# Kernel tuning notes

Hardware: AMD Instinct MI355X
Metric: run time of the kernel (lower is better)

The kernel has to match this reference:

```python
import jax, jax.numpy as jnp
import numpy as np
from jax import lax

AGG_HOPS = 3
RANK_K = 10
NEG = -1e9


def _aggregate(embs, agg_w, agg_b, W_last, b_last):
    # GIKT-style multi-hop mean aggregation: embs[j] has shape [B, n1..nj, D]
    embs = list(embs)
    for i in range(AGG_HOPS):
        for j in range(AGG_HOPS - i):
            s = jnp.mean(embs[j + 1], axis=-2) + embs[j]
            embs[j] = jnp.tanh(s @ agg_w[j].T + agg_b[j])
    return jnp.tanh(embs[0] @ W_last.T + b_last)


def _hops(nodes0, tabA, tabB):
    # alternating bipartite neighbor expansion: [B] -> [B,n] -> [B,n,n] -> ...
    lst = [nodes0]
    for i in range(AGG_HOPS):
        tab = tabA if i % 2 == 0 else tabB
        lst.append(tab[lst[-1]])
    return lst


def _forward(user, question, response, mask, q_neighbors, s_neighbors, u_neighbors,
             q_neighbors_2, qs_index, emb_question, emb_question_2, emb_skill,
             emb_user, emb_response, w1_q, w2_q, W_ih, W_hh, b_ih, b_hh,
             agg_w, agg_b, W_agg_last, b_agg_last, W_query, b_query, W_key, b_key,
             W_w, b_w, W_fusion, b_fusion):
    B, T = question.shape
    D = emb_question.shape[1]
    emb_q_all = emb_question[question]  # [B,T,D], used for recap similarity
    wA, wB = W_w[0, :D], W_w[0, D:]     # MLP_W(cat(Q,K)) = Q@wA + K@wB + b

    def predict(qs_concat, states, svalid):
        ql = (qs_concat @ W_query.T + b_query) @ wA          # [B,Lq]
        kl = (states @ W_key.T + b_key) @ wB                 # [B,Ls]
        logit = ql[:, :, None] + kl[:, None, :] + b_w[0]     # [B,Lq,Ls]
        logit = jnp.where(svalid[:, None, :], logit, NEG)
        Lq, Ls = logit.shape[1], logit.shape[2]
        alpha = jax.nn.softmax(logit.reshape(B, -1), axis=1).reshape(B, Lq, Ls)
        g = jnp.einsum('bqd,bsd->bqs', qs_concat, states)
        return jax.nn.sigmoid(jnp.sum(alpha * g, axis=(1, 2)))

    def step(carry, t):
        h, c, sh = carry
        q_t, u_t, r_t = question[:, t], user[:, t], response[:, t]
        m = (mask[:, t] == 1)[:, None]  # [B,1]
        # question-skill GNN branch
        embs_q = [(emb_question if i % 2 == 0 else emb_skill)[n]
                  for i, n in enumerate(_hops(q_t, q_neighbors, s_neighbors))]
        e1 = jnp.where(m, _aggregate(embs_q, agg_w, agg_b, W_agg_last, b_agg_last),
                       emb_question[q_t])
        # user-question GNN branch
        embs_u = [(emb_user if i % 2 == 0 else emb_question_2)[n]
                  for i, n in enumerate(_hops(u_t, u_neighbors, q_neighbors_2))]
        e2 = jnp.where(m, _aggregate(embs_u, agg_w, agg_b, W_agg_last, b_agg_last),
                       emb_question_2[q_t])
        e_hat = w1_q * e1 + w2_q * e2
        e_t = jax.nn.relu(jnp.concatenate([e_hat, emb_response[r_t]], axis=1)
                          @ W_fusion.T + b_fusion)
        # masked LSTMCell (torch gate order i,f,g,o); dropout in eval mode
        gates = e_t @ W_ih.T + b_ih + h @ W_hh.T + b_hh
        gi, gf, gg, go = jnp.split(gates, 4, axis=1)
        c2 = jax.nn.sigmoid(gf) * c + jax.nn.sigmoid(gi) * jnp.tanh(gg)
        h2 = jax.nn.sigmoid(go) * jnp.tanh(c2)
        h = jnp.where(m, h2, h)
        c = jnp.where(m, c2, c)
        sh = lax.dynamic_update_slice(sh, h[:, None, :], (0, t, 0))
        # next question + its related skills
        q_next = question[:, t + 1]
        emb_qn = emb_question[q_next]
        qs_concat = jnp.concatenate([emb_qn[:, None, :], emb_skill[qs_index[q_next]]], axis=1)
        # soft recap: top-k past states by (detached) question similarity
        scores = lax.stop_gradient(jnp.einsum('btd,bd->bt', emb_q_all, emb_qn))
        valid_t = jnp.arange(T) < t
        scores = jnp.where(valid_t[None, :], scores, NEG)
        _, idx = lax.top_k(scores, RANK_K)                    # [B,K]
        sel = jnp.take_along_axis(sh, idx[:, :, None], axis=1)  # [B,K,D]
        svalid = jnp.concatenate([jnp.ones((B, 1), bool), valid_t[idx]], axis=1)
        states = jnp.concatenate([h[:, None, :], sel], axis=1)  # [B,1+K,D]
        y = predict(qs_concat, states, svalid)
        return (h, c, sh), y

    h0 = jnp.zeros((B, D), jnp.float32)
    sh0 = jnp.zeros((B, T, D), jnp.float32)
    _, ys = lax.scan(step, (h0, h0, sh0), jnp.arange(T - 1))
    return jnp.concatenate([jnp.full((B, 1), 0.5, jnp.float32), ys.T], axis=1)


def setup_inputs() -> dict:
    B, T, D = 32, 50, 100
    NQ, NS, NU = 20000, 500, 10000
    NBR, SPQ = 6, 4
    key = jax.random.key(0)
    ks = iter(jax.random.split(key, 48))
    nrm = lambda shape, sc: jax.random.normal(next(ks), shape, jnp.float32) * sc
    ri = lambda shape, hi: jax.random.randint(next(ks), shape, 0, hi, jnp.int32)
    s = 1.0 / float(np.sqrt(D))
    return {
        'user': ri((B, T), NU), 'question': ri((B, T), NQ),
        'response': ri((B, T), 2), 'mask': ri((B, T), 2),
        'q_neighbors': ri((NQ, NBR), NS), 's_neighbors': ri((NS, NBR), NQ),
        'u_neighbors': ri((NU, NBR), NQ), 'q_neighbors_2': ri((NQ, NBR), NU),
        'qs_index': ri((NQ, SPQ), NS),
        'emb_question': nrm((NQ, D), 0.1), 'emb_question_2': nrm((NQ, D), 0.1),
        'emb_skill': nrm((NS, D), 0.1), 'emb_user': nrm((NU, D), 0.1),
        'emb_response': nrm((2, D), 0.1),
        'w1_q': jnp.float32(0.5), 'w2_q': jnp.float32(0.5),
        'W_ih': nrm((4 * D, D), s), 'W_hh': nrm((4 * D, D), s),
        'b_ih': jnp.zeros((4 * D,), jnp.float32), 'b_hh': jnp.zeros((4 * D,), jnp.float32),
        'agg_w': nrm((3, D, D), s), 'agg_b': jnp.zeros((3, D), jnp.float32),
        'W_agg_last': nrm((D, D), s), 'b_agg_last': jnp.zeros((D,), jnp.float32),
        'W_query': nrm((D, D), s), 'b_query': jnp.zeros((D,), jnp.float32),
        'W_key': nrm((D, D), s), 'b_key': jnp.zeros((D,), jnp.float32),
        'W_w': nrm((1, 2 * D), s), 'b_w': jnp.zeros((1,), jnp.float32),
        'W_fusion': nrm((D, 2 * D), s), 'b_fusion': jnp.zeros((D,), jnp.float32),
    }


def reference(user, question, response, mask, q_neighbors, s_neighbors, u_neighbors,
              q_neighbors_2, qs_index, emb_question, emb_question_2, emb_skill,
              emb_user, emb_response, w1_q, w2_q, W_ih, W_hh, b_ih, b_hh,
              agg_w, agg_b, W_agg_last, b_agg_last, W_query, b_query, W_key, b_key,
              W_w, b_w, W_fusion, b_fusion):
    return _forward(user, question, response, mask, q_neighbors, s_neighbors,
                    u_neighbors, q_neighbors_2, qs_index, emb_question,
                    emb_question_2, emb_skill, emb_user, emb_response, w1_q, w2_q,
                    W_ih, W_hh, b_ih, b_hh, agg_w, agg_b, W_agg_last, b_agg_last,
                    W_query, b_query, W_key, b_key, W_w, b_w, W_fusion, b_fusion)
```

## Files before the change

kernel.cpp:

```cpp
#include <hip/hip_runtime.h>
#include <hip/hip_bf16.h>

#define BSZ 32
#define TT 50
#define TS 49
#define PH 108

#define OFF_GPRE  0u
#define OFF_QL    627200u
#define OFF_IDX   639744u
#define OFF_NV    655424u
#define OFF_QSC   656992u
#define OFF_E1    1440992u
#define OFF_E2    1597792u

#define RLF(v,l) __uint_as_float(__builtin_amdgcn_readlane(__float_as_uint(v), (l)))

__device__ __forceinline__ float tanh_fast(float x) {
    float e = __expf(2.f * x);
    return 1.f - __fdividef(2.f, e + 1.f);
}
__device__ __forceinline__ float sigm_fast(float x) {
    return __fdividef(1.f, 1.f + __expf(-x));
}
__device__ __forceinline__ float dot4(float4 a, float4 b) {
    return a.x*b.x + a.y*b.y + a.z*b.z + a.w*b.w;
}

__global__ __launch_bounds__(256, 2) void kagg(
    const int* __restrict__ user, const int* __restrict__ question, const int* __restrict__ mask,
    const int* __restrict__ qnbr, const int* __restrict__ snbr,
    const int* __restrict__ unbr, const int* __restrict__ qnbr2,
    const float* __restrict__ embQ, const float* __restrict__ embQ2, const float* __restrict__ embS,
    const float* __restrict__ embU,
    const float* __restrict__ aggw, const float* __restrict__ aggb,
    const float* __restrict__ wlast, const float* __restrict__ blast,
    float* __restrict__ WS)
{
    int bid = blockIdx.x;
    int tid = threadIdx.x;

    int pair = bid >> 1, which = bid & 1;
    int b = pair / TS, t = pair - b*TS;
    int mm = mask[b*TT + t];
    float* outE = WS + (which ? OFF_E2 : OFF_E1) + (size_t)pair*100;

    if (mm != 1) {
        int q_t = question[b*TT + t];
        const float4* src = (const float4*)((which ? embQ2 : embQ) + (size_t)q_t*100);
        if (tid < 25) ((float4*)outE)[tid] = src[tid];
        return;
    }

    int root = which ? user[b*TT + t] : question[b*TT + t];
    const int*   tabA = which ? unbr  : qnbr;
    const int*   tabB = which ? qnbr2 : snbr;
    const float4* eE = (const float4*)(which ? embU  : embQ);
    const float4* eO = (const float4*)(which ? embQ2 : embS);

    __shared__ __align__(16) float b2in[36*108];
    __shared__ __align__(16) float x1[6*108];
    __shared__ float s2v1b[600];
    __shared__ float v1a[600];
    __shared__ __align__(16) float x0[104], v0a[104], v0b[104];
    __shared__ int n1[8], n2[36], n3[216];

    if (tid < 6) n1[tid] = tabA[root*6 + tid];
    __syncthreads();
    if (tid < 36) n2[tid] = tabB[n1[tid/6]*6 + (tid % 6)];
    __syncthreads();
    if (tid < 216) n3[tid] = tabA[n2[tid/6]*6 + (tid % 6)];
    __syncthreads();
    for (int i4 = tid; i4 < 900; i4 += 256) {
        int v = i4 / 25, j = i4 - v*25;
        float4 a = eE[(size_t)n2[v]*25 + j];
        float4 s = make_float4(0.f, 0.f, 0.f, 0.f);
        const int* p = n3 + v*6;
        #pragma unroll
        for (int c = 0; c < 6; ++c) {
            float4 o = eO[(size_t)p[c]*25 + j];
            s.x += o.x; s.y += o.y; s.z += o.z; s.w += o.w;
        }
        float4 r = make_float4(a.x + s.x*(1.f/6.f), a.y + s.y*(1.f/6.f),
                               a.z + s.z*(1.f/6.f), a.w + s.w*(1.f/6.f));
        *(float4*)(b2in + v*108 + 4*j) = r;
    }
    for (int i4 = tid; i4 < 150; i4 += 256) {
        int a = i4 / 25, j = i4 - a*25;
        float4 base = eO[(size_t)n1[a]*25 + j];
        float4 s = make_float4(0.f, 0.f, 0.f, 0.f);
        #pragma unroll
        for (int c = 0; c < 6; ++c) {
            float4 o = eE[(size_t)n2[a*6 + c]*25 + j];
            s.x += o.x; s.y += o.y; s.z += o.z; s.w += o.w;
        }
        float4 r = make_float4(base.x + s.x*(1.f/6.f), base.y + s.y*(1.f/6.f),
                               base.z + s.z*(1.f/6.f), base.w + s.w*(1.f/6.f));
        *(float4*)(x1 + a*108 + 4*j) = r;
    }
    if (tid >= 160 && tid < 185) {
        int j = tid - 160;
        float4 base = eE[(size_t)root*25 + j];
        float4 s = make_float4(0.f, 0.f, 0.f, 0.f);
        #pragma unroll
        for (int a = 0; a < 6; ++a) {
            float4 o = eO[(size_t)n1[a]*25 + j];
            s.x += o.x; s.y += o.y; s.z += o.z; s.w += o.w;
        }
        float4 r = make_float4(base.x + s.x*(1.f/6.f), base.y + s.y*(1.f/6.f),
                               base.z + s.z*(1.f/6.f), base.w + s.w*(1.f/6.f));
        *(float4*)(x0 + 4*j) = r;
    }
    __syncthreads();
    if (tid < 150) {
        int dblk = tid / 6, a = tid - dblk*6, d0 = dblk*4;
        const float* wp = aggw + 20000 + d0*100;
        const float* xb = b2in + a*648;
        float acc[4][6];
        #pragma unroll
        for (int r = 0; r < 4; ++r)
            #pragma unroll
            for (int c = 0; c < 6; ++c) acc[r][c] = 0.f;
        #pragma unroll
        for (int j = 0; j < 25; ++j) {
            float4 r0 = *(const float4*)(wp + 4*j);
            float4 r1 = *(const float4*)(wp + 100 + 4*j);
            float4 r2 = *(const float4*)(wp + 200 + 4*j);
            float4 r3 = *(const float4*)(wp + 300 + 4*j);
            #pragma unroll
            for (int c = 0; c < 6; ++c) {
                float4 x = *(const float4*)(xb + c*108 + 4*j);
                acc[0][c] += dot4(r0, x);
                acc[1][c] += dot4(r1, x);
                acc[2][c] += dot4(r2, x);
                acc[3][c] += dot4(r3, x);
            }
        }
        #pragma unroll
        for (int r = 0; r < 4; ++r) {
            float bia = aggb[200 + d0 + r];
            float o = 0.f;
            #pragma unroll
            for (int c = 0; c < 6; ++c) o += tanh_fast(bia + acc[r][c]);
            s2v1b[a*100 + d0 + r] = o;
        }
    } else if (tid >= 160 && tid < 210) {
        int d0 = (tid - 160)*2;
        const float* wp = aggw + 10000 + d0*100;
        float a0[6], a1[6];
        #pragma unroll
        for (int c = 0; c < 6; ++c) { a0[c] = 0.f; a1[c] = 0.f; }
        #pragma unroll
        for (int j = 0; j < 25; ++j) {
            float4 r0 = *(const float4*)(wp + 4*j);
            float4 r1 = *(const float4*)(wp + 100 + 4*j);
            #pragma unroll
            for (int c = 0; c < 6; ++c) {
                float4 x = *(const float4*)(x1 + c*108 + 4*j);
                a0[c] += dot4(r0, x);
                a1[c] += dot4(r1, x);
            }
        }
        #pragma unroll
        for (int c = 0; c < 6; ++c) {
            v1a[c*100 + d0]     = tanh_fast(aggb[100 + d0] + a0[c]);
            v1a[c*100 + d0 + 1] = tanh_fast(aggb[100 + d0 + 1] + a1[c]);
        }
    } else if (tid >= 216 && tid < 241) {
        int d0 = (tid - 216)*4;
        const float* wp = aggw + d0*100;
        float a0 = 0.f, a1 = 0.f, a2 = 0.f, a3 = 0.f;
        #pragma unroll
        for (int j = 0; j < 25; ++j) {
            float4 x = *(const float4*)(x0 + 4*j);
            a0 += dot4(*(const float4*)(wp + 4*j), x);
            a1 += dot4(*(const float4*)(wp + 100 + 4*j), x);
            a2 += dot4(*(const float4*)(wp + 200 + 4*j), x);
            a3 += dot4(*(const float4*)(wp + 300 + 4*j), x);
        }
        v0a[d0]   = tanh_fast(aggb[d0] + a0);
        v0a[d0+1] = tanh_fast(aggb[d0+1] + a1);
        v0a[d0+2] = tanh_fast(aggb[d0+2] + a2);
        v0a[d0+3] = tanh_fast(aggb[d0+3] + a3);
    }
    __syncthreads();
    for (int e = tid; e < 600; e += 256) {
        int a = e / 100, d = e - a*100;
        x1[a*108 + d] = v1a[a*100 + d] + s2v1b[a*100 + d]*(1.f/6.f);
    }
    if (tid >= 128 && tid < 228) {
        int d = tid - 128;
        float s = 0.f;
        #pragma unroll
        for (int a = 0; a < 6; ++a) s += v1a[a*100 + d];
        x0[d] = v0a[d] + s*(1.f/6.f);
    }
    __syncthreads();
    if (tid < 50) {
        int d0 = tid*2;
        const float* wp = aggw + 10000 + d0*100;
        float a0[6], a1[6];
        #pragma unroll
        for (int c = 0; c < 6; ++c) { a0[c] = 0.f; a1[c] = 0.f; }
        #pragma unroll
        for (int j = 0; j < 25; ++j) {
            float4 r0 = *(const float4*)(wp + 4*j);
            float4 r1 = *(const float4*)(wp + 100 + 4*j);
            #pragma unroll
            for (int c = 0; c < 6; ++c) {
                float4 x = *(const float4*)(x1 + c*108 + 4*j);
                a0[c] += dot4(r0, x);
                a1[c] += dot4(r1, x);
            }
        }
        #pragma unroll
        for (int c = 0; c < 6; ++c) {
            s2v1b[c*100 + d0]     = tanh_fast(aggb[100 + d0] + a0[c]);
            s2v1b[c*100 + d0 + 1] = tanh_fast(aggb[100 + d0 + 1] + a1[c]);
        }
    } else if (tid >= 64 && tid < 89) {
        int d0 = (tid - 64)*4;
        const float* wp = aggw + d0*100;
        float a0 = 0.f, a1 = 0.f, a2 = 0.f, a3 = 0.f;
        #pragma unroll
        for (int j = 0; j < 25; ++j) {
            float4 x = *(const float4*)(x0 + 4*j);
            a0 += dot4(*(const float4*)(wp + 4*j), x);
            a1 += dot4(*(const float4*)(wp + 100 + 4*j), x);
            a2 += dot4(*(const float4*)(wp + 200 + 4*j), x);
            a3 += dot4(*(const float4*)(wp + 300 + 4*j), x);
        }
        v0b[d0]   = tanh_fast(aggb[d0] + a0);
        v0b[d0+1] = tanh_fast(aggb[d0+1] + a1);
        v0b[d0+2] = tanh_fast(aggb[d0+2] + a2);
        v0b[d0+3] = tanh_fast(aggb[d0+3] + a3);
    }
    __syncthreads();
    if (tid < 100) {
        float s = 0.f;
        #pragma unroll
        for (int a = 0; a < 6; ++a) s += s2v1b[a*100 + tid];
        x0[tid] = v0b[tid] + s*(1.f/6.f);
    }
    __syncthreads();
    if (tid < 25) {
        int d0 = tid*4;
        const float* wp = aggw + d0*100;
        float a0 = 0.f, a1 = 0.f, a2 = 0.f, a3 = 0.f;
        #pragma unroll
        for (int j = 0; j < 25; ++j) {
            float4 x = *(const float4*)(x0 + 4*j);
            a0 += dot4(*(const float4*)(wp + 4*j), x);
            a1 += dot4(*(const float4*)(wp + 100 + 4*j), x);
            a2 += dot4(*(const float4*)(wp + 200 + 4*j), x);
            a3 += dot4(*(const float4*)(wp + 300 + 4*j), x);
        }
        v0a[d0]   = tanh_fast(aggb[d0] + a0);
        v0a[d0+1] = tanh_fast(aggb[d0+1] + a1);
        v0a[d0+2] = tanh_fast(aggb[d0+2] + a2);
        v0a[d0+3] = tanh_fast(aggb[d0+3] + a3);
    }
    __syncthreads();
    if (tid < 25) {
        int d0 = tid*4;
        const float* wp = wlast + d0*100;
        float a0 = 0.f, a1 = 0.f, a2 = 0.f, a3 = 0.f;
        #pragma unroll
        for (int j = 0; j < 25; ++j) {
            float4 x = *(const float4*)(v0a + 4*j);
            a0 += dot4(*(const float4*)(wp + 4*j), x);
            a1 += dot4(*(const float4*)(wp + 100 + 4*j), x);
            a2 += dot4(*(const float4*)(wp + 200 + 4*j), x);
            a3 += dot4(*(const float4*)(wp + 300 + 4*j), x);
        }
        float4 r = make_float4(tanh_fast(blast[d0] + a0), tanh_fast(blast[d0+1] + a1),
                               tanh_fast(blast[d0+2] + a2), tanh_fast(blast[d0+3] + a3));
        *(float4*)(outE + d0) = r;
    }
}

__global__ __launch_bounds__(256, 2) void kfuse(
    const int* __restrict__ question, const int* __restrict__ response,
    const int* __restrict__ qsidx,
    const float* __restrict__ embQ, const float* __restrict__ embS, const float* __restrict__ embR,
    const float* __restrict__ w1p, const float* __restrict__ w2p,
    const float* __restrict__ wfus, const float* __restrict__ bfus,
    const float* __restrict__ wih, const float* __restrict__ bih, const float* __restrict__ bhh,
    const float* __restrict__ wq, const float* __restrict__ bq, const float* __restrict__ ww,
    float* __restrict__ WS)
{
    int bid = blockIdx.x;
    int b = bid / TS, t = bid - b*TS;
    int tid = threadIdx.x;
    size_t bt = (size_t)b*TS + t;

    __shared__ __align__(16) float sEIN[200], sET[112], sEQN[104], sQSCm[500];
    __shared__ float sWW[104], sVQ[104], sScore[52], sCq[1];

    int r_t = response[b*TT + t];
    int qn  = question[b*TT + t + 1];
    if (tid < 100) {
        sEIN[tid] = w1p[0]*WS[OFF_E1 + bt*100 + tid] + w2p[0]*WS[OFF_E2 + bt*100 + tid];
    } else if (tid < 200) {
        sEIN[tid] = embR[r_t*100 + (tid - 100)];
        if (tid < 150) {
            int d = tid - 100;
            sEQN[d]      = embQ[(size_t)qn*100 + d];
            sEQN[d + 50] = embQ[(size_t)qn*100 + d + 50];
        }
    } else {
        for (int i = tid - 200; i < 100; i += 56) sWW[i] = ww[i];
    }
    __syncthreads();
    if (tid < 160) {
        int slot = tid >> 4, k0 = tid & 15;
        #pragma unroll
        for (int rp = 0; rp < 10; ++rp) {
            int row = rp*10 + slot;
            const float* wr = wfus + row*200;
            float acc = 0.f;
            #pragma unroll
            for (int m = 0; m < 4; ++m) {
                int f4i = k0 + 16*m;
                if (f4i < 50)
                    acc += dot4(*(const float4*)(wr + 4*f4i), *(const float4*)(sEIN + 4*f4i));
            }
            acc += __shfl_xor(acc, 1); acc += __shfl_xor(acc, 2);
            acc += __shfl_xor(acc, 4); acc += __shfl_xor(acc, 8);
            if (k0 == 0) sET[row] = fmaxf(acc + bfus[row], 0.f);
        }
    } else {
        for (int k = tid - 160; k < 100; k += 96) {
            float a = 0.f;
            for (int d = 0; d < 100; ++d) a += sWW[d] * wq[d*100 + k];
            sVQ[k] = a;
        }
        if (tid == 255) {
            float a = 0.f;
            for (int d = 0; d < 100; ++d) a += bq[d] * sWW[d];
            sCq[0] = a;
        }
    }
    __syncthreads();
    {
        int slot = tid >> 4, k0 = tid & 15;
        #pragma unroll 4
        for (int rp = 0; rp < 25; ++rp) {
            int row = rp*16 + slot;
            const float* wr = wih + row*100;
            float acc = 0.f;
            #pragma unroll
            for (int m = 0; m < 2; ++m) {
                int f4i = k0 + 16*m;
                if (f4i < 25)
                    acc += dot4(*(const float4*)(wr + 4*f4i), *(const float4*)(sET + 4*f4i));
            }
            acc += __shfl_xor(acc, 1); acc += __shfl_xor(acc, 2);
            acc += __shfl_xor(acc, 4); acc += __shfl_xor(acc, 8);
            if (k0 == 0) WS[OFF_GPRE + bt*400 + row] = acc + bih[row] + bhh[row];
        }
    }
    if (tid < 125) {
        int q = tid / 25, j = tid - q*25;
        float4 val = (q == 0) ? *(const float4*)(sEQN + 4*j)
                              : ((const float4*)embS)[(size_t)qsidx[qn*4 + (q-1)]*25 + j];
        *(float4*)(sQSCm + q*100 + 4*j) = val;
        *(float4*)(WS + OFF_QSC + bt*500 + q*100 + 4*j) = val;
    } else if (tid >= 128 && tid < 128 + TS) {
        int tp = tid - 128;
        if (tp < t) {
            int qq = question[b*TT + tp];
            const float* er = embQ + (size_t)qq*100;
            float acc = 0.f;
            #pragma unroll
            for (int k = 0; k < 25; ++k)
                acc += dot4(*(const float4*)(er + 4*k), *(const float4*)(sEQN + 4*k));
            sScore[tp] = acc;
        }
    }
    __syncthreads();
    if (tid < 80) {
        int q = tid >> 4, kk = tid & 15;
        float acc = 0.f;
        #pragma unroll
        for (int j = 0; j < 7; ++j) {
            int k = kk + 16*j;
            if (k < 100) acc = fmaf(sQSCm[q*100 + k], sVQ[k], acc);
        }
        acc += __shfl_xor(acc, 1); acc += __shfl_xor(acc, 2);
        acc += __shfl_xor(acc, 4); acc += __shfl_xor(acc, 8);
        if (kk == 0) WS[OFF_QL + bt*8 + q] = acc + sCq[0];
    }
    if (tid >= 128 && tid < 192) {
        int lane = tid - 128;
        int nv = t < 10 ? t : 10;
        int* idxp = (int*)(WS + OFF_IDX) + bt*10;
        if (lane == 0) ((int*)(WS + OFF_NV))[bt] = nv;
        float v = (lane < t) ? sScore[lane] : -3.0e38f;
        int myidx = lane;
        int taken = 0;
        for (int p = 0; p < 10; ++p) {
            float vv = taken ? -3.0e38f : v;
            int ii = myidx;
            #pragma unroll
            for (int m = 1; m < 64; m <<= 1) {
                float v2 = __shfl_xor(vv, m);
                int   i2 = __shfl_xor(ii, m);
                if (v2 > vv || (v2 == vv && i2 < ii)) { vv = v2; ii = i2; }
            }
            if (p < nv) {
                if (lane == 0) idxp[p] = ii;
                if (myidx == ii) taken = 1;
            } else if (lane == 0) idxp[p] = 0;
        }
    }
}

__global__ __launch_bounds__(576) void kseq(
    const int* __restrict__ mask, const float* __restrict__ whh,
    const float* __restrict__ wk, const float* __restrict__ bk,
    const float* __restrict__ ww, const float* __restrict__ bwp,
    const float* __restrict__ WS, float* __restrict__ out)
{
    int b = blockIdx.x, tid = threadIdx.x, lane = tid & 63;
    __shared__ __align__(16) float sQSCall[TS*500];
    __shared__ __align__(16) float sSH[TS*PH];
    __shared__ __align__(16) float sQLall[TS*8];
    __shared__ __align__(16) float sVKl[104];
    __shared__ int   sIdxAll[TS*10];
    __shared__ int   sNvAll[TS];
    __shared__ int   sMask[TT];
    __shared__ float sH[104], sC[104], sG[400];
    __shared__ float sKL2[2][12], sGv2[2][64];
    __shared__ float sCk[1];

    size_t b0 = (size_t)b*TS;
    int g = tid - 64;
    bool isGate = (g >= 0 && g < 400);

    float4 wv[25];
    if (isGate) {
        #pragma unroll
        for (int j = 0; j < 25; ++j) wv[j] = *(const float4*)(whh + g*100 + 4*j);
    }
    float gpre = isGate ? WS[OFF_GPRE + b0*400 + g] : 0.f;

    {
        const float4* src = (const float4*)(WS + OFF_QSC + b0*500);
        for (int i4 = tid; i4 < 6125; i4 += 576) ((float4*)sQSCall)[i4] = src[i4];
        const float4* srq = (const float4*)(WS + OFF_QL + b0*8);
        for (int i4 = tid; i4 < 98; i4 += 576) ((float4*)sQLall)[i4] = srq[i4];
    }
    for (int i = tid; i < TS*10;  i += 576) sIdxAll[i] = ((const int*)(WS + OFF_IDX))[b0*10 + i];
    for (int i = tid; i < TS;     i += 576) sNvAll[i]  = ((const int*)(WS + OFF_NV))[b0 + i];
    if (tid < TT) sMask[tid] = mask[b*TT + tid];
    if (tid < 104) { sH[tid] = 0.f; sC[tid] = 0.f; }
    if (tid >= 104 && tid < 204) {
        int k = tid - 104;
        float a = 0.f;
        for (int d = 0; d < 100; ++d) a += ww[100 + d] * wk[d*100 + k];
        sVKl[k] = a;
    }
    if (tid == 204) {
        float a = 0.f;
        for (int d = 0; d < 100; ++d) a += bk[d] * ww[100 + d];
        sCk[0] = a;
    }
    if (tid == 205) out[b*TT] = 0.5f;
    float bw = bwp[0];
    __syncthreads();
    float ck = sCk[0];

    for (int t = 0; t < TS; ++t) {
        int par = t & 1;
        float hA = sH[lane];
        float hB = sH[64 + (lane % 36)];
        if (isGate) {
            float gpre_nx = 0.f;
            if (t + 1 < TS) gpre_nx = WS[OFF_GPRE + (b0 + t + 1)*400 + g];
            float a0 = 0.f, a1 = 0.f, a2 = 0.f, a3 = 0.f;
            #pragma unroll
            for (int j = 0; j < 25; ++j) {
                const int kb = 4*j;
                float h0, h1, h2, h3;
                if (kb < 64) {
                    h0 = RLF(hA, kb);   h1 = RLF(hA, kb+1);
                    h2 = RLF(hA, kb+2); h3 = RLF(hA, kb+3);
                } else {
                    h0 = RLF(hB, kb-64); h1 = RLF(hB, kb-63);
                    h2 = RLF(hB, kb-62); h3 = RLF(hB, kb-61);
                }
                a0 = fmaf(h0, wv[j].x, a0);
                a1 = fmaf(h1, wv[j].y, a1);
                a2 = fmaf(h2, wv[j].z, a2);
                a3 = fmaf(h3, wv[j].w, a3);
            }
            sG[g] = (a0 + a1) + (a2 + a3) + gpre;
            gpre = gpre_nx;
        } else if (tid >= 512) {
            int nv = sNvAll[t];
            if (lane < 60) {
                bool isKL = lane < 10;
                int s = isKL ? (lane + 1) : (((lane - 10) % 10) + 1);
                int q = isKL ? 0 : ((lane - 10) / 10);
                if (s <= nv) {
                    const float* st = sSH + sIdxAll[t*10 + s - 1]*PH;
                    const float* xp = isKL ? sVKl : (sQSCall + t*500 + q*100);
                    float c0 = 0.f, c1 = 0.f, c2 = 0.f, c3 = 0.f;
                    #pragma unroll
                    for (int j = 0; j < 25; ++j) {
                        float4 a = *(const float4*)(st + 4*j);
                        float4 x = *(const float4*)(xp + 4*j);
                        c0 = fmaf(a.x, x.x, c0);
                        c1 = fmaf(a.y, x.y, c1);
                        c2 = fmaf(a.z, x.z, c2);
                        c3 = fmaf(a.w, x.w, c3);
                    }
                    float acc = (c0 + c1) + (c2 + c3);
                    if (isKL) sKL2[par][s] = acc + ck;
                    else      sGv2[par][q*12 + s] = acc;
                }
            }
        } else if (tid < 64 && t > 0) {
            int tau = t - 1, par2 = tau & 1;
            int nv = sNvAll[tau];
            int dd = lane >> 3, k0 = lane & 7;
            if (dd < 6) {
                const float* xp = (dd == 0) ? sVKl : (sQSCall + tau*500 + (dd-1)*100);
                float acc = 0.f;
                #pragma unroll
                for (int jj = 0; jj < 13; ++jj) {
                    int k = k0 + 8*jj;
                    if (k < 100) acc = fmaf(sH[k], xp[k], acc);
                }
                acc += __shfl_xor(acc, 1); acc += __shfl_xor(acc, 2); acc += __shfl_xor(acc, 4);
                if (k0 == 0) {
                    if (dd == 0) sKL2[par2][0] = acc + ck;
                    else         sGv2[par2][(dd-1)*12] = acc;
                }
            }
            int q = lane / 11, s = lane - q*11;
            bool valid = (lane < 55) && (s <= nv);
            float lg = valid ? (sQLall[tau*8 + q] + sKL2[par2][s] + bw) : 0.f;
            float e  = valid ? __expf(lg) : 0.f;
            float gv = valid ? sGv2[par2][q*12 + s] : 0.f;
            float se = e, sg = e*gv;
            #pragma unroll
            for (int m = 1; m < 64; m <<= 1) { se += __shfl_xor(se, m); sg += __shfl_xor(sg, m); }
            if (lane == 0) out[b*TT + tau + 1] = __fdividef(1.f, 1.f + __expf(-__fdividef(sg, se)));
        }
        __syncthreads();
        if (g >= 0 && g < 100) {
            float gi = sG[g], gf = sG[100+g], gg = sG[200+g], go = sG[300+g];
            float c2 = sigm_fast(gf)*sC[g] + sigm_fast(gi)*tanh_fast(gg);
            float h2 = sigm_fast(go)*tanh_fast(c2);
            if (sMask[t] == 1) { sH[g] = h2; sC[g] = c2; }
            sSH[t*PH + g] = sH[g];
        }
        __syncthreads();
    }
    if (tid < 64) {
        int tau = TS - 1, par2 = tau & 1;
        int nv = sNvAll[tau];
        int dd = lane >> 3, k0 = lane & 7;
        if (dd < 6) {
            const float* xp = (dd == 0) ? sVKl : (sQSCall + tau*500 + (dd-1)*100);
            float acc = 0.f;
            #pragma unroll
            for (int jj = 0; jj < 13; ++jj) {
                int k = k0 + 8*jj;
                if (k < 100) acc = fmaf(sH[k], xp[k], acc);
            }
            acc += __shfl_xor(acc, 1); acc += __shfl_xor(acc, 2); acc += __shfl_xor(acc, 4);
            if (k0 == 0) {
                if (dd == 0) sKL2[par2][0] = acc + ck;
                else         sGv2[par2][(dd-1)*12] = acc;
            }
        }
        int q = lane / 11, s = lane - q*11;
        bool valid = (lane < 55) && (s <= nv);
        float lg = valid ? (sQLall[tau*8 + q] + sKL2[par2][s] + bw) : 0.f;
        float e  = valid ? __expf(lg) : 0.f;
        float gv = valid ? sGv2[par2][q*12 + s] : 0.f;
        float se = e, sg = e*gv;
        #pragma unroll
        for (int m = 1; m < 64; m <<= 1) { se += __shfl_xor(se, m); sg += __shfl_xor(sg, m); }
        if (lane == 0) out[b*TT + tau + 1] = __fdividef(1.f, 1.f + __expf(-__fdividef(sg, se)));
    }
}

extern "C" void kernel_launch(void* const* d_in, const int* in_sizes, int n_in,
                              void* d_out, int out_size, void* d_ws, size_t ws_size,
                              hipStream_t stream) {
    const int* user      = (const int*)d_in[0];
    const int* question  = (const int*)d_in[1];
    const int* response  = (const int*)d_in[2];
    const int* mask      = (const int*)d_in[3];
    const int* qnbr      = (const int*)d_in[4];
    const int* snbr      = (const int*)d_in[5];
    const int* unbr      = (const int*)d_in[6];
    const int* qnbr2     = (const int*)d_in[7];
    const int* qsidx     = (const int*)d_in[8];
    const float* embQ    = (const float*)d_in[9];
    const float* embQ2   = (const float*)d_in[10];
    const float* embS    = (const float*)d_in[11];
    const float* embU    = (const float*)d_in[12];
    const float* embR    = (const float*)d_in[13];
    const float* w1      = (const float*)d_in[14];
    const float* w2      = (const float*)d_in[15];
    const float* wih     = (const float*)d_in[16];
    const float* whh     = (const float*)d_in[17];
    const float* bih     = (const float*)d_in[18];
    const float* bhh     = (const float*)d_in[19];
    const float* aggw    = (const float*)d_in[20];
    const float* aggb    = (const float*)d_in[21];
    const float* wlast   = (const float*)d_in[22];
    const float* blast   = (const float*)d_in[23];
    const float* wq      = (const float*)d_in[24];
    const float* bq      = (const float*)d_in[25];
    const float* wk      = (const float*)d_in[26];
    const float* bk      = (const float*)d_in[27];
    const float* ww      = (const float*)d_in[28];
    const float* bwp     = (const float*)d_in[29];
    const float* wfus    = (const float*)d_in[30];
    const float* bfus    = (const float*)d_in[31];
    float* WS = (float*)d_ws;
    float* out = (float*)d_out;

    hipLaunchKernelGGL(kagg, dim3(2*BSZ*TS), dim3(256), 0, stream,
                       user, question, mask, qnbr, snbr, unbr, qnbr2,
                       embQ, embQ2, embS, embU, aggw, aggb, wlast, blast, WS);
    hipLaunchKernelGGL(kfuse, dim3(BSZ*TS), dim3(256), 0, stream,
                       question, response, qsidx, embQ, embS, embR,
                       w1, w2, wfus, bfus, wih, bih, bhh, wq, bq, ww, WS);
    hipLaunchKernelGGL(kseq, dim3(BSZ), dim3(576), 0, stream,
                       mask, whh, wk, bk, ww, bwp, WS, out);
}
```

Baseline: 411.8 us.

## Precompute per-node neighbor-mean aggregates in a table pass before gathering

Adds a kernel that, for every question and every user, computes its own embedding plus the mean of its six neighbor embeddings and stores the result in workspace. The aggregation kernel then gathers these precomputed rows for hop-2 and root nodes, which removes the third neighbor-index lookup and the six-way gather-sum per node. This trades heavy redundant per-block gathers for one dense pass over the full tables, which may do unneeded work for nodes never visited. It also needs a larger workspace, and the new buffers overlap the regions kfuse uses later.

New measurement: 417.8 us. About the same (+1.5%).

```diff
diff --git a/kernel.cpp b/kernel.cpp
--- a/kernel.cpp
+++ b/kernel.cpp
@@ -6,13 +6,15 @@
 #define TS 49
 #define PH 108
 
+#define OFF_MAQ   0u
+#define OFF_MAU   2000000u
+#define OFF_E1    3000000u
+#define OFF_E2    3156800u
 #define OFF_GPRE  0u
 #define OFF_QL    627200u
 #define OFF_IDX   639744u
 #define OFF_NV    655424u
 #define OFF_QSC   656992u
-#define OFF_E1    1440992u
-#define OFF_E2    1597792u
 
 #define RLF(v,l) __uint_as_float(__builtin_amdgcn_readlane(__float_as_uint(v), (l)))
 
@@ -25,6 +27,43 @@
 }
 __device__ __forceinline__ float dot4(float4 a, float4 b) {
     return a.x*b.x + a.y*b.y + a.z*b.z + a.w*b.w;
+}
+
+__global__ __launch_bounds__(256) void kpre(
+    const int* __restrict__ qnbr, const int* __restrict__ unbr,
+    const float* __restrict__ embQ, const float* __restrict__ embS,
+    const float* __restrict__ embU, const float* __restrict__ embQ2,
+    float* __restrict__ WS)
+{
+    int idx = blockIdx.x*256 + threadIdx.x;
+    if (idx < 500000) {
+        int r = idx / 25, j = idx - r*25;
+        const int* nb = qnbr + r*6;
+        float4 a = ((const float4*)embQ)[(size_t)r*25 + j];
+        float4 s = make_float4(0.f, 0.f, 0.f, 0.f);
+        #pragma unroll
+        for (int c = 0; c < 6; ++c) {
+            float4 o = ((const float4*)embS)[(size_t)nb[c]*25 + j];
+            s.x += o.x; s.y += o.y; s.z += o.z; s.w += o.w;
+        }
+        float4 r4 = make_float4(a.x + s.x*(1.f/6.f), a.y + s.y*(1.f/6.f),
+                                a.z + s.z*(1.f/6.f), a.w + s.w*(1.f/6.f));
+        ((float4*)(WS + OFF_MAQ))[(size_t)r*25 + j] = r4;
+    } else if (idx < 750000) {
+        int i2 = idx - 500000;
+        int r = i2 / 25, j = i2 - r*25;
+        const int* nb = unbr + r*6;
+        float4 a = ((const float4*)embU)[(size_t)r*25 + j];
+        float4 s = make_float4(0.f, 0.f, 0.f, 0.f);
+        #pragma unroll
+        for (int c = 0; c < 6; ++c) {
+            float4 o = ((const float4*)embQ2)[(size_t)nb[c]*25 + j];
+            s.x += o.x; s.y += o.y; s.z += o.z; s.w += o.w;
+        }
+        float4 r4 = make_float4(a.x + s.x*(1.f/6.f), a.y + s.y*(1.f/6.f),
+                                a.z + s.z*(1.f/6.f), a.w + s.w*(1.f/6.f));
+        ((float4*)(WS + OFF_MAU))[(size_t)r*25 + j] = r4;
+    }
 }
 
 __global__ __launch_bounds__(256, 2) void kagg(
@@ -57,33 +96,22 @@
     const int*   tabB = which ? qnbr2 : snbr;
     const float4* eE = (const float4*)(which ? embU  : embQ);
     const float4* eO = (const float4*)(which ? embQ2 : embS);
+    const float4* MA = (const float4*)(WS + (which ? OFF_MAU : OFF_MAQ));
 
     __shared__ __align__(16) float b2in[36*108];
     __shared__ __align__(16) float x1[6*108];
     __shared__ float s2v1b[600];
     __shared__ float v1a[600];
     __shared__ __align__(16) float x0[104], v0a[104], v0b[104];
-    __shared__ int n1[8], n2[36], n3[216];
+    __shared__ int n1[8], n2[36];
 
     if (tid < 6) n1[tid] = tabA[root*6 + tid];
     __syncthreads();
     if (tid < 36) n2[tid] = tabB[n1[tid/6]*6 + (tid % 6)];
-    __syncthreads();
-    if (tid < 216) n3[tid] = tabA[n2[tid/6]*6 + (tid % 6)];
     __syncthreads();
     for (int i4 = tid; i4 < 900; i4 += 256) {
         int v = i4 / 25, j = i4 - v*25;
-        float4 a = eE[(size_t)n2[v]*25 + j];
-        float4 s = make_float4(0.f, 0.f, 0.f, 0.f);
-        const int* p = n3 + v*6;
-        #pragma unroll
-        for (int c = 0; c < 6; ++c) {
-            float4 o = eO[(size_t)p[c]*25 + j];
-            s.x += o.x; s.y += o.y; s.z += o.z; s.w += o.w;
-        }
-        float4 r = make_float4(a.x + s.x*(1.f/6.f), a.y + s.y*(1.f/6.f),
-                               a.z + s.z*(1.f/6.f), a.w + s.w*(1.f/6.f));
-        *(float4*)(b2in + v*108 + 4*j) = r;
+        *(float4*)(b2in + v*108 + 4*j) = MA[(size_t)n2[v]*25 + j];
     }
     for (int i4 = tid; i4 < 150; i4 += 256) {
         int a = i4 / 25, j = i4 - a*25;
@@ -100,16 +128,7 @@
     }
     if (tid >= 160 && tid < 185) {
         int j = tid - 160;
-        float4 base = eE[(size_t)root*25 + j];
-        float4 s = make_float4(0.f, 0.f, 0.f, 0.f);
-        #pragma unroll
-        for (int a = 0; a < 6; ++a) {
-            float4 o = eO[(size_t)n1[a]*25 + j];
-            s.x += o.x; s.y += o.y; s.z += o.z; s.w += o.w;
-        }
-        float4 r = make_float4(base.x + s.x*(1.f/6.f), base.y + s.y*(1.f/6.f),
-                               base.z + s.z*(1.f/6.f), base.w + s.w*(1.f/6.f));
-        *(float4*)(x0 + 4*j) = r;
+        *(float4*)(x0 + 4*j) = MA[(size_t)root*25 + j];
     }
     __syncthreads();
     if (tid < 150) {
@@ -627,6 +646,8 @@
     float* WS = (float*)d_ws;
     float* out = (float*)d_out;
 
+    hipLaunchKernelGGL(kpre, dim3((750000 + 255)/256), dim3(256), 0, stream,
+                       qnbr, unbr, embQ, embS, embU, embQ2, WS);
     hipLaunchKernelGGL(kagg, dim3(2*BSZ*TS), dim3(256), 0, stream,
                        user, question, mask, qnbr, snbr, unbr, qnbr2,
                        embQ, embQ2, embS, embU, aggw, aggb, wlast, blast, WS);
```
